# Kernel optimization log

Hardware: AMD Instinct MI355X
Metric: run time of the kernel (lower is better)

The kernel has to match this reference:

```python
import jax, jax.numpy as jnp
import numpy as np

B, T, E, H = 4, 2048, 4096, 128

def setup_inputs() -> dict:
    key = jax.random.key(0)
    ks = jax.random.split(key, 5)
    x = jax.random.normal(ks[0], (B, T, E), dtype=jnp.float32)
    pos_emb = jax.random.normal(ks[1], (B, T, E), dtype=jnp.float32)
    # torch nn.Linear(E, H, bias=False) weights have shape [H, E]
    scale = 1.0 / np.sqrt(E)
    Wq = jax.random.normal(ks[2], (H, E), dtype=jnp.float32) * scale
    Wk = jax.random.normal(ks[3], (H, E), dtype=jnp.float32) * scale
    Wv = jax.random.normal(ks[4], (H, E), dtype=jnp.float32) * scale
    return {"x": x, "pos_emb": pos_emb, "Wq": Wq, "Wk": Wk, "Wv": Wv}

def reference(x, pos_emb, Wq, Wk, Wv):
    Bd, Td, Ed = x.shape
    q = jnp.einsum('bte,he->bth', x, Wq)        # [B,T,H]
    k = jnp.einsum('bte,he->bth', pos_emb, Wk)  # [B,T,H] (key is computed from pos_emb, per source)
    v = jnp.einsum('bte,he->bth', x, Wv)        # [B,T,H]
    # NOTE: source scales by full model dim E**-0.5, not head_size**-0.5
    scores = jnp.einsum('bqh,bkh->bqk', q, k) * (Ed ** -0.5)  # [B,T,T]
    causal = jnp.tril(jnp.ones((Td, Td), dtype=bool))
    scores = jnp.where(causal[None, :, :], scores, -jnp.inf)
    attn = jax.nn.softmax(scores, axis=-1)
    out = jnp.einsum('bqk,bkh->bqh', attn, v)   # [B,T,H]
    return out
```

## Files before the change

kernel.cpp:

```cpp
#include <hip/hip_runtime.h>

#define BB 4
#define TT 2048
#define EE 4096
#define HH 128
#define MM (BB*TT)
#define SCALE 0.015625f

typedef short short8 __attribute__((ext_vector_type(8)));
typedef float f32x4 __attribute__((ext_vector_type(4)));
typedef unsigned short ushort_t;
typedef unsigned int u32;

__device__ __forceinline__ unsigned short f2bf(float x) {
    unsigned int u = __float_as_uint(x);
    u = (u + 0x7fffu + ((u >> 16) & 1u)) >> 16;
    return (unsigned short)u;
}

__global__ __launch_bounds__(256) void wconv(
    const float* __restrict__ Wq, const float* __restrict__ Wk,
    const float* __restrict__ Wv, ushort_t* __restrict__ Wb)
{
    const int gid = blockIdx.x * 256 + threadIdx.x;
    const int which = gid >> 16;
    const int rem = gid & 65535;
    const float* W = (which == 0) ? Wq : (which == 1) ? Wk : Wv;
    const float sc = (which == 0) ? SCALE : 1.0f;
    const float4 f0 = *(const float4*)(W + (size_t)rem * 8);
    const float4 f1 = *(const float4*)(W + (size_t)rem * 8 + 4);
    short8 pk;
    pk[0] = (short)f2bf(f0.x * sc); pk[1] = (short)f2bf(f0.y * sc);
    pk[2] = (short)f2bf(f0.z * sc); pk[3] = (short)f2bf(f0.w * sc);
    pk[4] = (short)f2bf(f1.x * sc); pk[5] = (short)f2bf(f1.y * sc);
    pk[6] = (short)f2bf(f1.z * sc); pk[7] = (short)f2bf(f1.w * sc);
    *(short8*)(Wb + (size_t)which * 524288 + (size_t)rem * 8) = pk;
}

#define KSPLIT 4
#define KSPAN  1024

__global__ __launch_bounds__(256, 3) void proj_mfma(
    const float* __restrict__ x, const float* __restrict__ pe,
    const ushort_t* __restrict__ Wb, float* __restrict__ Pp)
{
    const int mb   = blockIdx.x;
    const int widx = blockIdx.y;
    const int sp   = blockIdx.z;
    const float* in = (widx == 1) ? pe : x;
    const ushort_t* W = Wb + (size_t)widx * (128 * EE);

    const int tid  = threadIdx.x;
    const int lane = tid & 63, wave = tid >> 6;
    const int fr = lane & 15, quad = lane >> 4;

    const int rb    = mb * 128 + wave * 32;
    const int kbase = sp * KSPAN;

    f32x4 acc[2][8];
    #pragma unroll
    for (int m = 0; m < 2; m++)
        #pragma unroll
        for (int n = 0; n < 8; n++) acc[m][n] = (f32x4){0.f,0.f,0.f,0.f};

    const float* a0p = in + (size_t)(rb + fr) * EE + kbase + quad * 8;
    const float* a1p = in + (size_t)(rb + 16 + fr) * EE + kbase + quad * 8;
    const ushort_t* bp = W + (size_t)fr * EE + kbase + quad * 8;

    for (int kk = 0; kk < KSPAN; kk += 32) {
        const float4 x00 = *(const float4*)(a0p + kk);
        const float4 x01 = *(const float4*)(a0p + kk + 4);
        const float4 x10 = *(const float4*)(a1p + kk);
        const float4 x11 = *(const float4*)(a1p + kk + 4);
        short8 bf[8];
        #pragma unroll
        for (int n = 0; n < 8; n++)
            bf[n] = *(const short8*)(bp + (size_t)n * 16 * EE + kk);

        short8 af0, af1;
        af0[0]=(short)f2bf(x00.x); af0[1]=(short)f2bf(x00.y);
        af0[2]=(short)f2bf(x00.z); af0[3]=(short)f2bf(x00.w);
        af0[4]=(short)f2bf(x01.x); af0[5]=(short)f2bf(x01.y);
        af0[6]=(short)f2bf(x01.z); af0[7]=(short)f2bf(x01.w);
        af1[0]=(short)f2bf(x10.x); af1[1]=(short)f2bf(x10.y);
        af1[2]=(short)f2bf(x10.z); af1[3]=(short)f2bf(x10.w);
        af1[4]=(short)f2bf(x11.x); af1[5]=(short)f2bf(x11.y);
        af1[6]=(short)f2bf(x11.z); af1[7]=(short)f2bf(x11.w);

        #pragma unroll
        for (int n = 0; n < 8; n++) {
            acc[0][n] = __builtin_amdgcn_mfma_f32_16x16x32_bf16(af0, bf[n], acc[0][n], 0, 0, 0);
            acc[1][n] = __builtin_amdgcn_mfma_f32_16x16x32_bf16(af1, bf[n], acc[1][n], 0, 0, 0);
        }
    }

    float* P = Pp + ((size_t)(widx * KSPLIT + sp) * MM + rb) * HH;
    #pragma unroll
    for (int m = 0; m < 2; m++)
        #pragma unroll
        for (int n = 0; n < 8; n++)
            #pragma unroll
            for (int r = 0; r < 4; r++)
                P[(size_t)(m * 16 + quad * 4 + r) * HH + n * 16 + fr] = acc[m][n][r];
}

__global__ __launch_bounds__(256) void projcomb(
    const float* __restrict__ Pp,
    ushort_t* __restrict__ qo, ushort_t* __restrict__ ko_,
    ushort_t* __restrict__ vto)
{
    const int mb   = blockIdx.x;
    const int widx = blockIdx.y;
    const int tid  = threadIdx.x;
    const int m0 = mb * 64;
    const int r_ = tid >> 2;
    const int h0 = (tid & 3) * 32;

    __shared__ ushort_t T[128 * 72];

    const float* base = Pp + ((size_t)widx * KSPLIT * MM + m0 + r_) * HH + h0;
    float accv[32];
    #pragma unroll
    for (int j = 0; j < 8; j++) {
        float4 a = *(const float4*)(base + j * 4);
        accv[4*j+0] = a.x; accv[4*j+1] = a.y; accv[4*j+2] = a.z; accv[4*j+3] = a.w;
    }
    #pragma unroll
    for (int s = 1; s < KSPLIT; s++) {
        const float* bs = base + (size_t)s * MM * HH;
        #pragma unroll
        for (int j = 0; j < 8; j++) {
            float4 a = *(const float4*)(bs + j * 4);
            accv[4*j+0] += a.x; accv[4*j+1] += a.y;
            accv[4*j+2] += a.z; accv[4*j+3] += a.w;
        }
    }

    if (widx < 2) {
        ushort_t* out = (widx == 0) ? qo : ko_;
        #pragma unroll
        for (int j = 0; j < 4; j++) {
            short8 s_;
            #pragma unroll
            for (int e = 0; e < 8; e++) s_[e] = (short)f2bf(accv[j*8 + e]);
            *(short8*)&out[(size_t)(m0 + r_) * HH + h0 + j * 8] = s_;
        }
    } else {
        #pragma unroll
        for (int e = 0; e < 32; e++)
            T[(h0 + e) * 72 + r_] = f2bf(accv[e]);
        __syncthreads();
        const int h = tid >> 1, ms = (tid & 1) * 32;
        #pragma unroll
        for (int j = 0; j < 4; j++)
            *(short8*)&vto[(size_t)h * MM + m0 + ms + j * 8]
                = *(short8*)&T[h * 72 + ms + j * 8];
    }
}

__global__ __launch_bounds__(256) void attn_mfma(
    const ushort_t* __restrict__ qb, const ushort_t* __restrict__ kbf,
    const ushort_t* __restrict__ vtb,
    float* __restrict__ OP, float* __restrict__ LP)
{
    const int b = blockIdx.z;
    const int s = blockIdx.y;
    const int t = 63 - (int)blockIdx.x;
    const int tid  = threadIdx.x;
    const int lane = tid & 63, wave = tid >> 6;
    const int fr = lane & 15, quad = lane >> 4, ko = quad * 8;

    const int q0 = t * 32;
    const int C  = (t + 2) >> 1;
    const int cs = (C + 1) >> 1;
    const int c0 = s ? cs : 0;
    const int c1 = s ? C  : cs;

    __shared__ __align__(16) ushort_t Qs[32 * 136];
    __shared__ __align__(16) ushort_t Ks[64 * 136];
    __shared__ __align__(16) ushort_t Vt[128 * 72];
    __shared__ __align__(16) ushort_t Ps[32 * 72];
    __shared__ float lred[2][32];

    for (int f = tid; f < 512; f += 256) {
        const int row = f >> 4, sg = f & 15;
        *(short8*)&Qs[row * 136 + sg * 8] =
            *(const short8*)(qb + (size_t)(b * TT + q0 + row) * HH + sg * 8);
    }

    const int rhS = (wave & 1) * 16, cqS = (wave >> 1) * 32;
    const int rhO = (wave & 1) * 16, chO = (wave >> 1) * 64;

    f32x4 oacc[4];
    #pragma unroll
    for (int i = 0; i < 4; i++) oacc[i] = (f32x4){0.f,0.f,0.f,0.f};
    float lacc[4] = {0.f, 0.f, 0.f, 0.f};

    for (int c = c0; c < c1; c++) {
        const int kb_ = c * 64;
        for (int f = tid; f < 1024; f += 256) {
            const int row = f >> 4, sg = f & 15;
            *(short8*)&Ks[row * 136 + sg * 8] =
                *(const short8*)(kbf + (size_t)(b * TT + kb_ + row) * HH + sg * 8);
        }
        for (int f = tid; f < 1024; f += 256) {
            const int h = f >> 3, sg = f & 7;
            *(short8*)&Vt[h * 72 + sg * 8] =
                *(const short8*)(vtb + (size_t)h * MM + b * TT + kb_ + sg * 8);
        }
        __syncthreads();

        f32x4 sacc[2];
        sacc[0] = (f32x4){0.f,0.f,0.f,0.f};
        sacc[1] = (f32x4){0.f,0.f,0.f,0.f};
        #pragma unroll
        for (int kk = 0; kk < 128; kk += 32) {
            const short8 af = *(short8*)&Qs[(rhS + fr) * 136 + kk + ko];
            const short8 b0 = *(short8*)&Ks[(cqS + fr) * 136 + kk + ko];
            const short8 b1 = *(short8*)&Ks[(cqS + 16 + fr) * 136 + kk + ko];
            sacc[0] = __builtin_amdgcn_mfma_f32_16x16x32_bf16(af, b0, sacc[0], 0, 0, 0);
            sacc[1] = __builtin_amdgcn_mfma_f32_16x16x32_bf16(af, b1, sacc[1], 0, 0, 0);
        }

        #pragma unroll
        for (int tl = 0; tl < 2; tl++)
            #pragma unroll
            for (int r = 0; r < 4; r++) {
                const int row = rhS + quad * 4 + r;
                const int col = cqS + tl * 16 + fr;
                const float p = ((kb_ + col) <= (q0 + row)) ? __expf(sacc[tl][r]) : 0.f;
                lacc[r] += p;
                Ps[row * 72 + col] = f2bf(p);
            }
        __syncthreads();

        #pragma unroll
        for (int ks = 0; ks < 64; ks += 32) {
            const short8 af = *(short8*)&Ps[(rhO + fr) * 72 + ks + ko];
            #pragma unroll
            for (int tl = 0; tl < 4; tl++) {
                const short8 bf_ = *(short8*)&Vt[(chO + tl * 16 + fr) * 72 + ks + ko];
                oacc[tl] = __builtin_amdgcn_mfma_f32_16x16x32_bf16(af, bf_, oacc[tl], 0, 0, 0);
            }
        }
        __syncthreads();
    }

    #pragma unroll
    for (int r = 0; r < 4; r++) {
        float v = lacc[r];
        #pragma unroll
        for (int m = 1; m < 16; m <<= 1) v += __shfl_xor(v, m);
        lacc[r] = v;
    }
    if (fr == 0) {
        #pragma unroll
        for (int r = 0; r < 4; r++)
            lred[wave >> 1][rhS + quad * 4 + r] = lacc[r];
    }
    __syncthreads();
    const int pbase = ((b * 64 + t) * 2 + s);
    if (tid < 32) LP[(size_t)pbase * 32 + tid] = lred[0][tid] + lred[1][tid];

    #pragma unroll
    for (int tl = 0; tl < 4; tl++)
        #pragma unroll
        for (int r = 0; r < 4; r++) {
            const int row = rhO + quad * 4 + r;
            const int col = chO + tl * 16 + fr;
            OP[(size_t)pbase * 4096 + row * 128 + col] = oacc[tl][r];
        }
}

__global__ __launch_bounds__(256) void combine(
    const float* __restrict__ OP, const float* __restrict__ LP,
    float* __restrict__ out)
{
    const int gid = blockIdx.x * 256 + threadIdx.x;
    const int b = gid >> 16;
    const int rem = gid & 65535;
    const int qrow = rem >> 5, h4 = rem & 31;
    const int t = qrow >> 5, r = qrow & 31;
    const int base = (b * 64 + t) * 2;
    const float l = LP[(size_t)base * 32 + r] + LP[(size_t)(base + 1) * 32 + r];
    const float inv = 1.f / l;
    const float4 a = ((const float4*)OP)[(size_t)base * 1024 + r * 32 + h4];
    const float4 c = ((const float4*)OP)[(size_t)(base + 1) * 1024 + r * 32 + h4];
    float4 res;
    res.x = (a.x + c.x) * inv; res.y = (a.y + c.y) * inv;
    res.z = (a.z + c.z) * inv; res.w = (a.w + c.w) * inv;
    ((float4*)out)[gid] = res;
}

extern "C" void kernel_launch(void* const* d_in, const int* in_sizes, int n_in,
                              void* d_out, int out_size, void* d_ws, size_t ws_size,
                              hipStream_t stream) {
    const float* x  = (const float*)d_in[0];
    const float* pe = (const float*)d_in[1];
    const float* Wq = (const float*)d_in[2];
    const float* Wk = (const float*)d_in[3];
    const float* Wv = (const float*)d_in[4];
    float* out = (float*)d_out;

    ushort_t* qb  = (ushort_t*)d_ws;
    ushort_t* kbf = qb  + (size_t)MM * HH;
    ushort_t* vtb = kbf + (size_t)MM * HH;
    ushort_t* Wb  = vtb + (size_t)MM * HH;
    float* Pp = (float*)(Wb + (size_t)3 * 128 * 4096);
    float* OP = Pp;
    float* LP = OP + (size_t)512 * 4096;

    wconv    <<<768, 256, 0, stream>>>(Wq, Wk, Wv, Wb);
    proj_mfma<<<dim3(64, 3, KSPLIT), 256, 0, stream>>>(x, pe, Wb, Pp);
    projcomb <<<dim3(128, 3), 256, 0, stream>>>(Pp, qb, kbf, vtb);
    attn_mfma<<<dim3(64, 2, BB), 256, 0, stream>>>(qb, kbf, vtb, OP, LP);
    combine  <<<1024, 256, 0, stream>>>(OP, LP, out);
}
```

Measured before the change: 420.1 us.

## Stage projection GEMM tiles through LDS with async global_load_lds double buffering

The projection kernel now loads 128x32 fp32 input tiles and 128x32 bf16 weight tiles into shared memory with direct global-to-LDS loads. It double-buffers them across K steps and uses an XOR swizzle to avoid bank conflicts. Each wave computes a 64x64 sub-tile instead of a 32x128 strip, so B fragments are shared from LDS rather than re-fetched from global memory by every wave. This cuts redundant global/L2 traffic and overlaps loads with MFMA, at the cost of more LDS use and a barrier per step, which may reduce occupancy.

```diff
diff --git a/kernel.cpp b/kernel.cpp
--- a/kernel.cpp
+++ b/kernel.cpp
@@ -16,6 +16,12 @@
     unsigned int u = __float_as_uint(x);
     u = (u + 0x7fffu + ((u >> 16) & 1u)) >> 16;
     return (unsigned short)u;
+}
+
+__device__ __forceinline__ void gl_lds16(const void* g, void* l) {
+    __builtin_amdgcn_global_load_lds(
+        (const __attribute__((address_space(1))) u32*)g,
+        (__attribute__((address_space(3))) u32*)l, 16, 0, 0);
 }
 
 __global__ __launch_bounds__(256) void wconv(
@@ -39,6 +45,8 @@
 
 #define KSPLIT 4
 #define KSPAN  1024
+#define BK     32
+#define NSTEPS (KSPAN / BK)
 
 __global__ __launch_bounds__(256, 3) void proj_mfma(
     const float* __restrict__ x, const float* __restrict__ pe,
@@ -50,58 +58,92 @@
     const float* in = (widx == 1) ? pe : x;
     const ushort_t* W = Wb + (size_t)widx * (128 * EE);
 
+    const int rb    = mb * 128;
+    const int kbase = sp * KSPAN;
+
     const int tid  = threadIdx.x;
     const int lane = tid & 63, wave = tid >> 6;
+    const int wr = wave & 1, wc = wave >> 1;
     const int fr = lane & 15, quad = lane >> 4;
 
-    const int rb    = mb * 128 + wave * 32;
-    const int kbase = sp * KSPAN;
-
-    f32x4 acc[2][8];
-    #pragma unroll
-    for (int m = 0; m < 2; m++)
-        #pragma unroll
-        for (int n = 0; n < 8; n++) acc[m][n] = (f32x4){0.f,0.f,0.f,0.f};
-
-    const float* a0p = in + (size_t)(rb + fr) * EE + kbase + quad * 8;
-    const float* a1p = in + (size_t)(rb + 16 + fr) * EE + kbase + quad * 8;
-    const ushort_t* bp = W + (size_t)fr * EE + kbase + quad * 8;
-
-    for (int kk = 0; kk < KSPAN; kk += 32) {
-        const float4 x00 = *(const float4*)(a0p + kk);
-        const float4 x01 = *(const float4*)(a0p + kk + 4);
-        const float4 x10 = *(const float4*)(a1p + kk);
-        const float4 x11 = *(const float4*)(a1p + kk + 4);
-        short8 bf[8];
-        #pragma unroll
-        for (int n = 0; n < 8; n++)
-            bf[n] = *(const short8*)(bp + (size_t)n * 16 * EE + kk);
-
-        short8 af0, af1;
-        af0[0]=(short)f2bf(x00.x); af0[1]=(short)f2bf(x00.y);
-        af0[2]=(short)f2bf(x00.z); af0[3]=(short)f2bf(x00.w);
-        af0[4]=(short)f2bf(x01.x); af0[5]=(short)f2bf(x01.y);
-        af0[6]=(short)f2bf(x01.z); af0[7]=(short)f2bf(x01.w);
-        af1[0]=(short)f2bf(x10.x); af1[1]=(short)f2bf(x10.y);
-        af1[2]=(short)f2bf(x10.z); af1[3]=(short)f2bf(x10.w);
-        af1[4]=(short)f2bf(x11.x); af1[5]=(short)f2bf(x11.y);
-        af1[6]=(short)f2bf(x11.z); af1[7]=(short)f2bf(x11.w);
-
-        #pragma unroll
-        for (int n = 0; n < 8; n++) {
-            acc[0][n] = __builtin_amdgcn_mfma_f32_16x16x32_bf16(af0, bf[n], acc[0][n], 0, 0, 0);
-            acc[1][n] = __builtin_amdgcn_mfma_f32_16x16x32_bf16(af1, bf[n], acc[1][n], 0, 0, 0);
-        }
-    }
+    __shared__ __align__(16) float    As[2][128 * BK];
+    __shared__ __align__(16) ushort_t Bs[2][128 * BK];
+
+    f32x4 acc[4][4];
+    #pragma unroll
+    for (int m = 0; m < 4; m++)
+        #pragma unroll
+        for (int n = 0; n < 4; n++) acc[m][n] = (f32x4){0.f,0.f,0.f,0.f};
+
+    const int a_row = tid >> 3;
+    const int a_sw  = (((tid & 7) * 16) ^ ((a_row & 7) << 4)) >> 2;
+    const float* a_src = in + (size_t)(rb + a_row) * EE + kbase + a_sw;
+
+    const int b_row = tid >> 2;
+    const int b_sw  = (((tid & 3) * 16) ^ ((b_row & 3) << 4)) >> 1;
+    const ushort_t* b_src = W + (size_t)b_row * EE + kbase + b_sw;
+
+#define STAGE(K0, BUF) do { \
+    _Pragma("unroll") \
+    for (int j_ = 0; j_ < 4; j_++) \
+        gl_lds16(a_src + (size_t)j_ * 32 * EE + (K0), \
+                 &As[BUF][j_ * 1024 + tid * 4]); \
+    _Pragma("unroll") \
+    for (int r_ = 0; r_ < 2; r_++) \
+        gl_lds16(b_src + (size_t)r_ * 64 * EE + (K0), \
+                 &Bs[BUF][r_ * 2048 + tid * 8]); \
+} while (0)
+
+    const int ac0 = ((quad * 32)      ^ ((fr & 7) << 4)) >> 2;
+    const int ac1 = ((quad * 32 + 16) ^ ((fr & 7) << 4)) >> 2;
+    const int bc0 = ((quad * 16)      ^ ((fr & 3) << 4)) >> 1;
+
+    STAGE(0, 0);
+    __syncthreads();
+
+    for (int s = 0; s < NSTEPS; s++) {
+        const int buf = s & 1;
+        if (s + 1 < NSTEPS) STAGE((s + 1) * BK, buf ^ 1);
+
+        short8 bfr[4];
+        #pragma unroll
+        for (int n = 0; n < 4; n++)
+            bfr[n] = *(short8*)&Bs[buf][(wc * 64 + n * 16 + fr) * BK + bc0];
+
+        short8 afr[4];
+        #pragma unroll
+        for (int m = 0; m < 4; m++) {
+            const int arow = (wr * 64 + m * 16 + fr) * BK;
+            const f32x4 c0 = *(f32x4*)&As[buf][arow + ac0];
+            const f32x4 c1 = *(f32x4*)&As[buf][arow + ac1];
+            short8 a_;
+            a_[0]=(short)f2bf(c0[0]); a_[1]=(short)f2bf(c0[1]);
+            a_[2]=(short)f2bf(c0[2]); a_[3]=(short)f2bf(c0[3]);
+            a_[4]=(short)f2bf(c1[0]); a_[5]=(short)f2bf(c1[1]);
+            a_[6]=(short)f2bf(c1[2]); a_[7]=(short)f2bf(c1[3]);
+            afr[m] = a_;
+        }
+
+        #pragma unroll
+        for (int m = 0; m < 4; m++)
+            #pragma unroll
+            for (int n = 0; n < 4; n++)
+                acc[m][n] = __builtin_amdgcn_mfma_f32_16x16x32_bf16(
+                    afr[m], bfr[n], acc[m][n], 0, 0, 0);
+
+        __syncthreads();
+    }
+#undef STAGE
 
     float* P = Pp + ((size_t)(widx * KSPLIT + sp) * MM + rb) * HH;
     #pragma unroll
-    for (int m = 0; m < 2; m++)
-        #pragma unroll
-        for (int n = 0; n < 8; n++)
+    for (int m = 0; m < 4; m++)
+        #pragma unroll
+        for (int n = 0; n < 4; n++)
             #pragma unroll
             for (int r = 0; r < 4; r++)
-                P[(size_t)(m * 16 + quad * 4 + r) * HH + n * 16 + fr] = acc[m][n][r];
+                P[(size_t)(wr * 64 + m * 16 + quad * 4 + r) * HH
+                  + wc * 64 + n * 16 + fr] = acc[m][n][r];
 }
 
 __global__ __launch_bounds__(256) void projcomb(
```

Result: faster. 376.5 us (-10.4%).
